# Optimization experiments

Measured on AMD Instinct MI355X. Metric: run time of the kernel, lower is better.

## Reference

```python
import jax, jax.numpy as jnp
import numpy as np

B, R, C, H, W = 4, 2, 19, 256, 512


def setup_inputs() -> dict:
    key = jax.random.key(0)
    k1, k2, k3 = jax.random.split(key, 3)
    return {
        "ref_pred": jax.random.normal(k1, (B, R, C, H, W), dtype=jnp.float32),
        # motion vectors in quarter-pel units (divided by 4 inside forward);
        # scale so displacements span a few pixels
        "ref_mv": jax.random.normal(k2, (B, R, 2, H, W), dtype=jnp.float32) * 8.0,
        "ref_weight": jax.random.uniform(k3, (B, R, 1, H, W), dtype=jnp.float32),
    }


def _warp(img, mv):
    """Bilinear backward warp (grid_sample, zeros padding).
    img: [N, C, H, W], mv: [N, 2, H, W] pixel displacements (x, y)."""
    N, Ch, Hh, Ww = img.shape
    ys, xs = jnp.meshgrid(jnp.arange(Hh, dtype=mv.dtype),
                          jnp.arange(Ww, dtype=mv.dtype), indexing="ij")
    gx = xs + mv[:, 0]  # [N, H, W] sample x-coordinate
    gy = ys + mv[:, 1]  # [N, H, W] sample y-coordinate
    x0 = jnp.floor(gx); y0 = jnp.floor(gy)
    x1 = x0 + 1.0;      y1 = y0 + 1.0
    wx1 = gx - x0; wx0 = 1.0 - wx1
    wy1 = gy - y0; wy0 = 1.0 - wy1

    img_flat = img.reshape(N, Ch, Hh * Ww)

    def samp(iy, ix):
        valid = ((ix >= 0) & (ix <= Ww - 1) & (iy >= 0) & (iy <= Hh - 1))
        iyc = jnp.clip(iy, 0, Hh - 1).astype(jnp.int32)
        ixc = jnp.clip(ix, 0, Ww - 1).astype(jnp.int32)
        lin = (iyc * Ww + ixc).reshape(N, 1, Hh * Ww)
        vals = jnp.take_along_axis(
            img_flat, jnp.broadcast_to(lin, (N, Ch, Hh * Ww)), axis=2
        ).reshape(N, Ch, Hh, Ww)
        return vals * valid.astype(img.dtype)[:, None]

    out = (samp(y0, x0) * (wy0 * wx0)[:, None]
           + samp(y0, x1) * (wy0 * wx1)[:, None]
           + samp(y1, x0) * (wy1 * wx0)[:, None]
           + samp(y1, x1) * (wy1 * wx1)[:, None])
    return out


def reference(ref_pred, ref_mv, ref_weight):
    Bb, Rr = ref_pred.shape[:2]
    pred = ref_pred.reshape(Bb * Rr, *ref_pred.shape[2:])   # [B*R, C, H, W]
    mv = ref_mv.reshape(Bb * Rr, *ref_mv.shape[2:]) / 4.0    # quarter-pel -> pixel
    # eval mode, eval_noise_sigma=0 -> no noise added
    warped = _warp(pred, mv)                                  # [B*R, C, H, W]
    w = ref_weight.reshape(Bb * Rr, *ref_weight.shape[2:])   # [B*R, 1, H, W]
    warped = warped * w
    return warped.reshape(Bb, Rr, *warped.shape[1:]).sum(axis=1)  # [B, C, H, W]
```

## Files before the change

kernel.cpp:

```cpp
#include <hip/hip_runtime.h>

constexpr int B = 4, R = 2, C = 19, H = 256, W = 512;
constexpr int HW = H * W;

constexpr int BX = 64, BY = 16;
constexpr int NBX = W / BX;
constexpr int NBY = H / BY;
constexpr int NSPAT = B * NBX * NBY;

constexpr int TW = 92;
constexpr int TH = 42;
constexpr int TILE_N = TW * TH;
constexpr int TILE_V4 = TILE_N / 4;

#define GLD_LDS16(gsrc, ldst)                                                  \
    __builtin_amdgcn_global_load_lds(                                          \
        (const __attribute__((address_space(1))) void*)(gsrc),                 \
        (__attribute__((address_space(3))) void*)(ldst), 16, 0, 0)

__global__ __launch_bounds__(256, 4) void mc_warp_kernel(
    const float* __restrict__ pred,
    const float* __restrict__ mv,
    const float* __restrict__ wgt,
    float* __restrict__ out)
{
    __shared__ float tile0[TILE_N];
    __shared__ float tile1[TILE_N];

    int t = threadIdx.x;
    int xcd  = blockIdx.x & 7;
    int slot = blockIdx.x >> 3;
    int vblk = xcd * (NSPAT / 8) + slot;
    int bx   = vblk & (NBX - 1);
    int by   = (vblk >> 3) & (NBY - 1);
    int b    = vblk >> 7;
    int x0 = bx * BX, y0 = by * BY;
    int tx = t & 15, ty = t >> 4;
    int y  = y0 + ty;
    int xb = x0 + tx * 4;

    int rowbase = min(max(y0 - 12, 0), H - TH);
    int colbase = min(max(x0 - 12, 0), W - TW);

    const float* pl0 = pred + (size_t)(b * R + 0) * C * HW;
    const float* pl1 = pred + (size_t)(b * R + 1) * C * HW;
    const float* st0 = pl0 + (size_t)rowbase * W + colbase;
    const float* st1 = pl1 + (size_t)rowbase * W + colbase;

    int cbeg = (blockIdx.y == 0) ? 0 : 10;
    int cend = (blockIdx.y == 0) ? 10 : 19;

    {
        const float* s0 = st0 + (size_t)cbeg * HW;
        const float* s1 = st1 + (size_t)cbeg * HW;
        #pragma unroll
        for (int i = 0; i < 4; ++i) {
            int idx = t + i * 256;
            if (idx < TILE_V4) {
                int row = idx / 23;
                int off = idx * 4 + row * (W - TW);
                GLD_LDS16(s0 + off, &tile0[idx * 4]);
                GLD_LDS16(s1 + off, &tile1[idx * 4]);
            }
        }
    }

    int   off0[R][4], off1[R][4];
    int   offL0[R][4], offL1[R][4], offG0[R][4], offG1[R][4];
    float wq[R][4][4];
    int flag = 0;

    #pragma unroll
    for (int r = 0; r < R; ++r) {
        const float* mvp = mv + (size_t)((b * R + r) * 2) * HW + (size_t)y * W + xb;
        float4 mx4 = *(const float4*)(mvp);
        float4 my4 = *(const float4*)(mvp + HW);
        float4 wr4 = *(const float4*)(wgt + (size_t)(b * R + r) * HW + (size_t)y * W + xb);
        float mxs[4] = {mx4.x, mx4.y, mx4.z, mx4.w};
        float mys[4] = {my4.x, my4.y, my4.z, my4.w};
        float wrs[4] = {wr4.x, wr4.y, wr4.z, wr4.w};
        #pragma unroll
        for (int p = 0; p < 4; ++p) {
            int x = xb + p;
            float gx = (float)x + mxs[p] * 0.25f;
            float gy = (float)y + mys[p] * 0.25f;
            float fx0 = floorf(gx), fy0 = floorf(gy);
            float wx1 = gx - fx0, wx0 = 1.0f - wx1;
            float wy1 = gy - fy0, wy0 = 1.0f - wy1;
            int ix0 = (int)fx0, iy0 = (int)fy0;
            int ix1 = ix0 + 1,  iy1 = iy0 + 1;

            int base = min(max(ix0, 0), W - 2);
            float wA = (ix0 == base)     ? wx0 : ((ix1 == base)     ? wx1 : 0.0f);
            float wB = (ix1 == base + 1) ? wx1 : ((ix0 == base + 1) ? wx0 : 0.0f);
            float wr = wrs[p];
            float wy0v = ((iy0 >= 0) && (iy0 < H)) ? wy0 * wr : 0.0f;
            float wy1v = ((iy1 >= 0) && (iy1 < H)) ? wy1 * wr : 0.0f;
            int cy0 = min(max(iy0, 0), H - 1);
            int cy1 = min(max(iy1, 0), H - 1);

            int l0 = base - colbase;
            int r0 = cy0 - rowbase, r1 = cy1 - rowbase;
            bool anyx = (wA != 0.0f) || (wB != 0.0f);
            bool anyy = (wy0v != 0.0f) || (wy1v != 0.0f);
            bool cb  = (l0 < 0 || l0 > TW - 2) && anyx && anyy;
            bool rb0 = (r0 < 0 || r0 > TH - 1) && (wy0v != 0.0f) && anyx;
            bool rb1 = (r1 < 0 || r1 > TH - 1) && (wy1v != 0.0f) && anyx;
            flag |= (int)(cb || rb0 || rb1);
            l0 = min(max(l0, 0), TW - 2);
            r0 = min(max(r0, 0), TH - 1);
            r1 = min(max(r1, 0), TH - 1);

            offL0[r][p] = r0 * TW + l0;
            offL1[r][p] = r1 * TW + l0;
            offG0[r][p] = cy0 * W + base;
            offG1[r][p] = cy1 * W + base;
            wq[r][p][0] = wy0v * wA;
            wq[r][p][1] = wy0v * wB;
            wq[r][p][2] = wy1v * wA;
            wq[r][p][3] = wy1v * wB;
        }
    }

    int fbB = __syncthreads_or(flag);
    #pragma unroll
    for (int r = 0; r < R; ++r)
        #pragma unroll
        for (int p = 0; p < 4; ++p) {
            off0[r][p] = fbB ? offG0[r][p] : offL0[r][p];
            off1[r][p] = fbB ? offG1[r][p] : offL1[r][p];
        }

    float* ob = out + (size_t)b * C * HW + (size_t)y * W + xb;

    for (int c = cbeg; c < cend; ++c) {
        if (c > cbeg) {
            __syncthreads();
            if (!fbB) {
                const float* s0 = st0 + (size_t)c * HW;
                const float* s1 = st1 + (size_t)c * HW;
                #pragma unroll
                for (int i = 0; i < 4; ++i) {
                    int idx = t + i * 256;
                    if (idx < TILE_V4) {
                        int row = idx / 23;
                        int off = idx * 4 + row * (W - TW);
                        GLD_LDS16(s0 + off, &tile0[idx * 4]);
                        GLD_LDS16(s1 + off, &tile1[idx * 4]);
                    }
                }
            }
        }
        __syncthreads();

        float res[4];
        if (!fbB) {
            #pragma unroll
            for (int p = 0; p < 4; ++p) {
                float a00 = tile0[off0[0][p]], a01 = tile0[off0[0][p] + 1];
                float a10 = tile0[off1[0][p]], a11 = tile0[off1[0][p] + 1];
                float b00 = tile1[off0[1][p]], b01 = tile1[off0[1][p] + 1];
                float b10 = tile1[off1[1][p]], b11 = tile1[off1[1][p] + 1];
                res[p] = wq[0][p][0] * a00 + wq[0][p][1] * a01
                       + wq[0][p][2] * a10 + wq[0][p][3] * a11
                       + wq[1][p][0] * b00 + wq[1][p][1] * b01
                       + wq[1][p][2] * b10 + wq[1][p][3] * b11;
            }
        } else {
            const float* pc0 = pl0 + (size_t)c * HW;
            const float* pc1 = pl1 + (size_t)c * HW;
            #pragma unroll
            for (int p = 0; p < 4; ++p) {
                float a00 = pc0[off0[0][p]], a01 = pc0[off0[0][p] + 1];
                float a10 = pc0[off1[0][p]], a11 = pc0[off1[0][p] + 1];
                float b00 = pc1[off0[1][p]], b01 = pc1[off0[1][p] + 1];
                float b10 = pc1[off1[1][p]], b11 = pc1[off1[1][p] + 1];
                res[p] = wq[0][p][0] * a00 + wq[0][p][1] * a01
                       + wq[0][p][2] * a10 + wq[0][p][3] * a11
                       + wq[1][p][0] * b00 + wq[1][p][1] * b01
                       + wq[1][p][2] * b10 + wq[1][p][3] * b11;
            }
        }
        *(float4*)(ob + (size_t)c * HW) = make_float4(res[0], res[1], res[2], res[3]);
    }
}

extern "C" void kernel_launch(void* const* d_in, const int* in_sizes, int n_in,
                              void* d_out, int out_size, void* d_ws, size_t ws_size,
                              hipStream_t stream) {
    const float* pred = (const float*)d_in[0];
    const float* mv   = (const float*)d_in[1];
    const float* wgt  = (const float*)d_in[2];
    float* out = (float*)d_out;

    dim3 grid(NSPAT, 2);
    mc_warp_kernel<<<grid, dim3(256), 0, stream>>>(pred, mv, wgt, out);
}
```

Baseline: 152.6 us.

## Split channels into four chunks, shrink halo tile, stride pixels across lanes

Splits the channel loop over four grid slices instead of two and shrinks the LDS halo tile (92x42 to 88x37), raising the launch-bounds occupancy target from 4 to 6 blocks per CU. Each thread now handles pixels strided by 16 instead of four contiguous ones, so LDS gathers across a wavefront are spread over more columns and global stores/loads become scalar but coalesced. The smaller halo makes the global-memory fallback path more likely, and more channel chunks mean the mv/weight setup and tile halo loads are repeated more often.

Result: slower. 244.9 us (+60.5%).

```diff
diff --git a/kernel.cpp b/kernel.cpp
--- a/kernel.cpp
+++ b/kernel.cpp
@@ -7,9 +7,10 @@
 constexpr int NBX = W / BX;
 constexpr int NBY = H / BY;
 constexpr int NSPAT = B * NBX * NBY;
-
-constexpr int TW = 92;
-constexpr int TH = 42;
+constexpr int NCHUNK = 4;
+
+constexpr int TW = 88;
+constexpr int TH = 37;
 constexpr int TILE_N = TW * TH;
 constexpr int TILE_V4 = TILE_N / 4;
 
@@ -18,7 +19,7 @@
         (const __attribute__((address_space(1))) void*)(gsrc),                 \
         (__attribute__((address_space(3))) void*)(ldst), 16, 0, 0)
 
-__global__ __launch_bounds__(256, 4) void mc_warp_kernel(
+__global__ __launch_bounds__(256, 6) void mc_warp_kernel(
     const float* __restrict__ pred,
     const float* __restrict__ mv,
     const float* __restrict__ wgt,
@@ -37,9 +38,9 @@
     int x0 = bx * BX, y0 = by * BY;
     int tx = t & 15, ty = t >> 4;
     int y  = y0 + ty;
-    int xb = x0 + tx * 4;
-
-    int rowbase = min(max(y0 - 12, 0), H - TH);
+    int xb = x0 + tx;
+
+    int rowbase = min(max(y0 - 10, 0), H - TH);
     int colbase = min(max(x0 - 12, 0), W - TW);
 
     const float* pl0 = pred + (size_t)(b * R + 0) * C * HW;
@@ -47,8 +48,8 @@
     const float* st0 = pl0 + (size_t)rowbase * W + colbase;
     const float* st1 = pl1 + (size_t)rowbase * W + colbase;
 
-    int cbeg = (blockIdx.y == 0) ? 0 : 10;
-    int cend = (blockIdx.y == 0) ? 10 : 19;
+    int cbeg = (C * blockIdx.y) / NCHUNK;
+    int cend = (C * (blockIdx.y + 1)) / NCHUNK;
 
     {
         const float* s0 = st0 + (size_t)cbeg * HW;
@@ -57,7 +58,7 @@
         for (int i = 0; i < 4; ++i) {
             int idx = t + i * 256;
             if (idx < TILE_V4) {
-                int row = idx / 23;
+                int row = idx / 22;
                 int off = idx * 4 + row * (W - TW);
                 GLD_LDS16(s0 + off, &tile0[idx * 4]);
                 GLD_LDS16(s1 + off, &tile1[idx * 4]);
@@ -72,16 +73,19 @@
 
     #pragma unroll
     for (int r = 0; r < R; ++r) {
-        const float* mvp = mv + (size_t)((b * R + r) * 2) * HW + (size_t)y * W + xb;
-        float4 mx4 = *(const float4*)(mvp);
-        float4 my4 = *(const float4*)(mvp + HW);
-        float4 wr4 = *(const float4*)(wgt + (size_t)(b * R + r) * HW + (size_t)y * W + xb);
-        float mxs[4] = {mx4.x, mx4.y, mx4.z, mx4.w};
-        float mys[4] = {my4.x, my4.y, my4.z, my4.w};
-        float wrs[4] = {wr4.x, wr4.y, wr4.z, wr4.w};
+        const float* mvxp = mv + (size_t)((b * R + r) * 2) * HW + (size_t)y * W + xb;
+        const float* mvyp = mvxp + HW;
+        const float* wp   = wgt + (size_t)(b * R + r) * HW + (size_t)y * W + xb;
+        float mxs[4], mys[4], wrs[4];
         #pragma unroll
         for (int p = 0; p < 4; ++p) {
-            int x = xb + p;
+            mxs[p] = mvxp[16 * p];
+            mys[p] = mvyp[16 * p];
+            wrs[p] = wp[16 * p];
+        }
+        #pragma unroll
+        for (int p = 0; p < 4; ++p) {
+            int x = xb + 16 * p;
             float gx = (float)x + mxs[p] * 0.25f;
             float gy = (float)y + mys[p] * 0.25f;
             float fx0 = floorf(gx), fy0 = floorf(gy);
@@ -143,7 +147,7 @@
                 for (int i = 0; i < 4; ++i) {
                     int idx = t + i * 256;
                     if (idx < TILE_V4) {
-                        int row = idx / 23;
+                        int row = idx / 22;
                         int off = idx * 4 + row * (W - TW);
                         GLD_LDS16(s0 + off, &tile0[idx * 4]);
                         GLD_LDS16(s1 + off, &tile1[idx * 4]);
@@ -181,7 +185,10 @@
                        + wq[1][p][2] * b10 + wq[1][p][3] * b11;
             }
         }
-        *(float4*)(ob + (size_t)c * HW) = make_float4(res[0], res[1], res[2], res[3]);
+        float* oc = ob + (size_t)c * HW;
+        #pragma unroll
+        for (int p = 0; p < 4; ++p)
+            oc[16 * p] = res[p];
     }
 }
 
@@ -193,6 +200,6 @@
     const float* wgt  = (const float*)d_in[2];
     float* out = (float*)d_out;
 
-    dim3 grid(NSPAT, 2);
+    dim3 grid(NSPAT, NCHUNK);
     mc_warp_kernel<<<grid, dim3(256), 0, stream>>>(pred, mv, wgt, out);
 }
```

## Double-buffer LDS channel tiles and split channels into four grid chunks

Applied to the files above, without the earlier changes.

Loads the next channel's source tile into a second LDS buffer while the current channel is interpolated, so global-to-LDS transfer overlaps compute. The halo tile shrinks to 88x37 and the channel range is split across four grid slices instead of two. More blocks run in parallel, at the cost of recomputing motion vectors and weights per block and doubling LDS per block. The smaller halo also sends more pixels to the slow global fallback path.

Measured after the change: 150.9 us. No clear change (-1.1%).

```diff
diff --git a/kernel.cpp b/kernel.cpp
--- a/kernel.cpp
+++ b/kernel.cpp
@@ -7,9 +7,10 @@
 constexpr int NBX = W / BX;
 constexpr int NBY = H / BY;
 constexpr int NSPAT = B * NBX * NBY;
+constexpr int NCHUNK = 4;
 
-constexpr int TW = 92;
-constexpr int TH = 42;
+constexpr int TW = 88;
+constexpr int TH = 37;
 constexpr int TILE_N = TW * TH;
 constexpr int TILE_V4 = TILE_N / 4;
 
@@ -24,8 +25,7 @@
     const float* __restrict__ wgt,
     float* __restrict__ out)
 {
-    __shared__ float tile0[TILE_N];
-    __shared__ float tile1[TILE_N];
+    __shared__ float tiles[2][2][TILE_N];
 
     int t = threadIdx.x;
     int xcd  = blockIdx.x & 7;
@@ -39,7 +39,7 @@
     int y  = y0 + ty;
     int xb = x0 + tx * 4;
 
-    int rowbase = min(max(y0 - 12, 0), H - TH);
+    int rowbase = min(max(y0 - 10, 0), H - TH);
     int colbase = min(max(x0 - 12, 0), W - TW);
 
     const float* pl0 = pred + (size_t)(b * R + 0) * C * HW;
@@ -47,8 +47,8 @@
     const float* st0 = pl0 + (size_t)rowbase * W + colbase;
     const float* st1 = pl1 + (size_t)rowbase * W + colbase;
 
-    int cbeg = (blockIdx.y == 0) ? 0 : 10;
-    int cend = (blockIdx.y == 0) ? 10 : 19;
+    int cbeg = (C * blockIdx.y) / NCHUNK;
+    int cend = (C * (blockIdx.y + 1)) / NCHUNK;
 
     {
         const float* s0 = st0 + (size_t)cbeg * HW;
@@ -57,10 +57,10 @@
         for (int i = 0; i < 4; ++i) {
             int idx = t + i * 256;
             if (idx < TILE_V4) {
-                int row = idx / 23;
+                int row = idx / 22;
                 int off = idx * 4 + row * (W - TW);
-                GLD_LDS16(s0 + off, &tile0[idx * 4]);
-                GLD_LDS16(s1 + off, &tile1[idx * 4]);
+                GLD_LDS16(s0 + off, &tiles[0][0][idx * 4]);
+                GLD_LDS16(s1 + off, &tiles[0][1][idx * 4]);
             }
         }
     }
@@ -133,34 +133,35 @@
 
     float* ob = out + (size_t)b * C * HW + (size_t)y * W + xb;
 
-    for (int c = cbeg; c < cend; ++c) {
-        if (c > cbeg) {
-            __syncthreads();
-            if (!fbB) {
-                const float* s0 = st0 + (size_t)c * HW;
-                const float* s1 = st1 + (size_t)c * HW;
-                #pragma unroll
-                for (int i = 0; i < 4; ++i) {
-                    int idx = t + i * 256;
-                    if (idx < TILE_V4) {
-                        int row = idx / 23;
-                        int off = idx * 4 + row * (W - TW);
-                        GLD_LDS16(s0 + off, &tile0[idx * 4]);
-                        GLD_LDS16(s1 + off, &tile1[idx * 4]);
-                    }
+    int cur = 0;
+    for (int c = cbeg; c < cend; ++c, cur ^= 1) {
+        __syncthreads();
+
+        if (!fbB && c + 1 < cend) {
+            const float* s0 = st0 + (size_t)(c + 1) * HW;
+            const float* s1 = st1 + (size_t)(c + 1) * HW;
+            #pragma unroll
+            for (int i = 0; i < 4; ++i) {
+                int idx = t + i * 256;
+                if (idx < TILE_V4) {
+                    int row = idx / 22;
+                    int off = idx * 4 + row * (W - TW);
+                    GLD_LDS16(s0 + off, &tiles[cur ^ 1][0][idx * 4]);
+                    GLD_LDS16(s1 + off, &tiles[cur ^ 1][1][idx * 4]);
                 }
             }
         }
-        __syncthreads();
 
         float res[4];
         if (!fbB) {
+            const float* tb0 = &tiles[cur][0][0];
+            const float* tb1 = &tiles[cur][1][0];
             #pragma unroll
             for (int p = 0; p < 4; ++p) {
-                float a00 = tile0[off0[0][p]], a01 = tile0[off0[0][p] + 1];
-                float a10 = tile0[off1[0][p]], a11 = tile0[off1[0][p] + 1];
-                float b00 = tile1[off0[1][p]], b01 = tile1[off0[1][p] + 1];
-                float b10 = tile1[off1[1][p]], b11 = tile1[off1[1][p] + 1];
+                float a00 = tb0[off0[0][p]], a01 = tb0[off0[0][p] + 1];
+                float a10 = tb0[off1[0][p]], a11 = tb0[off1[0][p] + 1];
+                float b00 = tb1[off0[1][p]], b01 = tb1[off0[1][p] + 1];
+                float b10 = tb1[off1[1][p]], b11 = tb1[off1[1][p] + 1];
                 res[p] = wq[0][p][0] * a00 + wq[0][p][1] * a01
                        + wq[0][p][2] * a10 + wq[0][p][3] * a11
                        + wq[1][p][0] * b00 + wq[1][p][1] * b01
@@ -193,6 +194,6 @@
     const float* wgt  = (const float*)d_in[2];
     float* out = (float*)d_out;
 
-    dim3 grid(NSPAT, 2);
+    dim3 grid(NSPAT, NCHUNK);
     mc_warp_kernel<<<grid, dim3(256), 0, stream>>>(pred, mv, wgt, out);
 }
```
